# Performance work log

Hardware: AMD Instinct MI355X
Metric: run time of the kernel (lower is better)

The kernel has to match this reference:

```python
import jax, jax.numpy as jnp
import numpy as np

D_MODEL = 1024
N_HEADS = 16
D_K = D_MODEL // N_HEADS
D_FF = 4096
EPS = 1e-6


def _layernorm(x, g, b):
    mu = jnp.mean(x, axis=-1, keepdims=True)
    var = jnp.mean(jnp.square(x - mu), axis=-1, keepdims=True)
    return (x - mu) * jax.lax.rsqrt(var + EPS) * g + b


def setup_inputs() -> dict:
    key = jax.random.key(0)
    ks = jax.random.split(key, 12)
    B, S = 2, 2048
    sd_attn = (1.0 / np.sqrt(2.0)) * np.sqrt(2.0 / (D_MODEL + D_MODEL))  # xavier gain 1/sqrt(2) (std approx)
    sd_ff1 = np.sqrt(2.0 / (D_MODEL + D_FF))
    sd_ff2 = np.sqrt(2.0 / (D_FF + D_MODEL))
    return {
        "x": jax.random.normal(ks[0], (B, S, D_MODEL), jnp.float32),
        "mask": jnp.ones((B, S), jnp.int32),
        # weights stored (in, out) so forward is x @ W
        "wq": jax.random.normal(ks[1], (D_MODEL, D_MODEL), jnp.float32) * sd_attn,
        "wk": jax.random.normal(ks[2], (D_MODEL, D_MODEL), jnp.float32) * sd_attn,
        "wv": jax.random.normal(ks[3], (D_MODEL, D_MODEL), jnp.float32) * sd_attn,
        "wo": jax.random.normal(ks[4], (D_MODEL, D_MODEL), jnp.float32) * sd_attn,
        "wo_b": jnp.zeros((D_MODEL,), jnp.float32),
        "w1": jax.random.normal(ks[5], (D_MODEL, D_FF), jnp.float32) * sd_ff1,
        "b1": jnp.zeros((D_FF,), jnp.float32),
        "w2": jax.random.normal(ks[6], (D_FF, D_MODEL), jnp.float32) * sd_ff2,
        "b2": jnp.zeros((D_MODEL,), jnp.float32),
        "g1": jnp.ones((D_MODEL,), jnp.float32),
        "be1": jnp.zeros((D_MODEL,), jnp.float32),
        "g2": jnp.ones((D_MODEL,), jnp.float32),
        "be2": jnp.zeros((D_MODEL,), jnp.float32),
    }


def reference(x, mask, wq, wk, wv, wo, wo_b, w1, b1, w2, b2, g1, be1, g2, be2):
    B, S, _ = x.shape
    scale = 1.0 / np.sqrt(D_K)
    # project and split heads -> [B, H, S, Dk]
    q = (x @ wq).reshape(B, S, N_HEADS, D_K).transpose(0, 2, 1, 3)
    k = (x @ wk).reshape(B, S, N_HEADS, D_K).transpose(0, 2, 1, 3)
    v = (x @ wv).reshape(B, S, N_HEADS, D_K).transpose(0, 2, 1, 3)
    scores = jnp.einsum("bhqd,bhkd->bhqk", q, k) * scale  # [B,H,S,S]
    m = (mask[:, None, None, :] == 0)
    scores = jnp.where(m, -1e9, scores)
    attn = jax.nn.softmax(scores, axis=-1)
    ctx = jnp.einsum("bhqk,bhkd->bhqd", attn, v)
    ctx = ctx.transpose(0, 2, 1, 3).reshape(B, S, D_MODEL)
    attn_out = ctx @ wo + wo_b
    x = _layernorm(x + attn_out, g1, be1)
    ff = jax.nn.gelu(x @ w1 + b1, approximate=False) @ w2 + b2
    return _layernorm(x + ff, g2, be2)
```

## Files before the change

kernel.cpp:

```cpp
#include <hip/hip_runtime.h>
#include <cstdint>

#define DEVINL __device__ __forceinline__

typedef __attribute__((ext_vector_type(8))) short short8;
typedef __attribute__((ext_vector_type(4))) short short4v;
typedef __attribute__((ext_vector_type(4))) float floatx4;
typedef __attribute__((ext_vector_type(4))) unsigned short ushort4v;

DEVINL uint32_t pkbf(float a, float b) {
  uint32_t d;
  asm("v_cvt_pk_bf16_f32 %0, %1, %2" : "=v"(d) : "v"(a), "v"(b));
  return d;
}
DEVINL unsigned short f2bf(float f) {
  union { float f; uint32_t u; } v; v.f = f;
  return (unsigned short)((v.u + 0x7fffu + ((v.u >> 16) & 1u)) >> 16);
}
DEVINL float bf2f(unsigned short h) {
  union { uint32_t u; float f; } v; v.u = ((uint32_t)h) << 16;
  return v.f;
}

#if defined(__has_builtin) && __has_builtin(__builtin_amdgcn_exp2f)
#define EXP2(x) __builtin_amdgcn_exp2f(x)
#else
#define EXP2(x) exp2f(x)
#endif

DEVINL float fast_gelu(float v) {
  const float z = -2.30220795f * v * (1.0f + 0.044715f * v * v);
  return v * __builtin_amdgcn_rcpf(1.0f + EXP2(z));
}

typedef __attribute__((address_space(3))) unsigned char* lds_ptr_t;
typedef const __attribute__((address_space(1))) unsigned char* gbl_ptr_t;
DEVINL void load_lds_128(const void* g, void* l) {
  __builtin_amdgcn_global_load_lds((gbl_ptr_t)g, (lds_ptr_t)l, 16, 0, 0);
}

#define MFMA16(a, b, c) __builtin_amdgcn_mfma_f32_16x16x32_bf16((a), (b), (c), 0, 0, 0)

#define QSCALE2 0.18033688011112042f

__global__ __launch_bounds__(256) void prep_kernel(
    const float* __restrict__ x, unsigned short* __restrict__ XB,
    const float* __restrict__ wq, const float* __restrict__ wk,
    const float* __restrict__ wv, const float* __restrict__ wo,
    unsigned short* __restrict__ WQKV, unsigned short* __restrict__ WOT,
    const float* __restrict__ w1, unsigned short* __restrict__ W1T,
    const float* __restrict__ w2, unsigned short* __restrict__ W2T,
    const int* __restrict__ mask, unsigned short* __restrict__ MB) {
  const int bid = blockIdx.x;
  if (bid >= 16384) {
    const int i0 = threadIdx.x * 16;
#pragma unroll
    for (int j = 0; j < 16; ++j) MB[i0 + j] = mask[i0 + j] ? 0x3F80 : 0;
    return;
  }
  if (bid < 4096) {
    const int i = (bid * 256 + threadIdx.x) * 4;
    floatx4 v = *(const floatx4*)(x + i);
    union { uint32_t u[2]; ushort4v v4; } o;
    o.u[0] = pkbf(v[0], v[1]);
    o.u[1] = pkbf(v[2], v[3]);
    *(ushort4v*)(XB + i) = o.v4;
    return;
  }
  const float* in;
  unsigned short* out;
  int K, N, bx, by;
  if (bid < 8192) {
    const int b2 = bid - 4096, z = b2 >> 10;
    in = (z == 0) ? wq : (z == 1) ? wk : (z == 2) ? wv : wo;
    out = (z == 3) ? WOT : WQKV + (size_t)z * 1024 * 1024;
    K = 1024; N = 1024; bx = b2 & 31; by = (b2 >> 5) & 31;
  } else if (bid < 12288) {
    const int b3 = bid - 8192;
    in = w1; out = W1T; K = 1024; N = 4096; bx = b3 & 127; by = b3 >> 7;
  } else {
    const int b4 = bid - 12288;
    in = w2; out = W2T; K = 4096; N = 1024; bx = b4 & 31; by = b4 >> 5;
  }
  __shared__ float tile[32][33];
  const int n0 = bx * 32, k0 = by * 32;
  const int tx = threadIdx.x & 31, ty = threadIdx.x >> 5;
#pragma unroll
  for (int i = 0; i < 4; ++i)
    tile[ty + 8 * i][tx] = in[(size_t)(k0 + ty + 8 * i) * N + n0 + tx];
  __syncthreads();
#pragma unroll
  for (int i = 0; i < 4; ++i)
    out[(size_t)(n0 + ty + 8 * i) * K + k0 + tx] = f2bf(tile[tx][ty + 8 * i]);
}

template <int EPI, int SK>
__global__ __launch_bounds__(256) void gemm_bt_kernel(
    const unsigned short* __restrict__ A, const unsigned short* __restrict__ BT,
    const float* __restrict__ bias, void* __restrict__ C0, void* __restrict__ C1,
    void* __restrict__ C2, int M, int N, int K, const int* __restrict__ msk) {
  __shared__ __align__(16) unsigned short As[128 * 64];
  __shared__ __align__(16) unsigned short Bs[128 * 64];
  const int tid = threadIdx.x;
  const int w = tid >> 6, l = tid & 63;
  const int lq = l >> 4, lr = l & 15;
  const int m0 = blockIdx.y * 128, n0 = blockIdx.x * 128;
  const int wm = (w >> 1) * 64, wn = (w & 1) * 64;
  const int r_a = l >> 2;
  const int colb = (l & 3) * 8;
  const int kslice = K / SK;
  const int kbeg = kslice * blockIdx.z;
  const int region = (EPI == 5) ? (n0 >> 10) : 0;

  uint32_t mbits = 0xFFFFu;
  if (EPI == 5 && region == 2) {
    mbits = 0;
#pragma unroll
    for (int mt = 0; mt < 4; ++mt) {
      const int4 m4 = *(const int4*)(msk + m0 + wm + mt * 16 + lq * 4);
      mbits |= (m4.x ? 1u : 0u) << (mt * 4);
      mbits |= (m4.y ? 1u : 0u) << (mt * 4 + 1);
      mbits |= (m4.z ? 1u : 0u) << (mt * 4 + 2);
      mbits |= (m4.w ? 1u : 0u) << (mt * 4 + 3);
    }
  }

  floatx4 acc[4][4];
  const floatx4 fz = {0.f, 0.f, 0.f, 0.f};
#pragma unroll
  for (int mt = 0; mt < 4; ++mt)
#pragma unroll
    for (int nt = 0; nt < 4; ++nt) acc[mt][nt] = fz;

  for (int k0 = kbeg; k0 < kbeg + kslice; k0 += 64) {
    __syncthreads();
#pragma unroll
    for (int p = 0; p < 2; ++p) {
#pragma unroll
      for (int i = 0; i < 2; ++i) {
        const int c = w * 2 + i;
        load_lds_128(A + (size_t)(m0 + c * 16 + r_a) * K + k0 + p * 32 + colb,
                     (char*)As + p * 8192 + c * 1024);
        load_lds_128(BT + (size_t)(n0 + c * 16 + r_a) * K + k0 + p * 32 + colb,
                     (char*)Bs + p * 8192 + c * 1024);
      }
    }
    __syncthreads();
#pragma unroll
    for (int p = 0; p < 2; ++p) {
      short8 af[4], bf[4];
#pragma unroll
      for (int mt = 0; mt < 4; ++mt)
        af[mt] = *(const short8*)((const char*)As + p * 8192 + (wm + mt * 16 + lr) * 64 + lq * 16);
#pragma unroll
      for (int nt = 0; nt < 4; ++nt)
        bf[nt] = *(const short8*)((const char*)Bs + p * 8192 + (wn + nt * 16 + lr) * 64 + lq * 16);
#pragma unroll
      for (int mt = 0; mt < 4; ++mt)
#pragma unroll
        for (int nt = 0; nt < 4; ++nt)
          acc[mt][nt] = MFMA16(af[mt], bf[nt], acc[mt][nt]);
    }
  }

  void* Cp = (SK > 1 && blockIdx.z) ? C1 : C0;
#pragma unroll
  for (int mt = 0; mt < 4; ++mt) {
#pragma unroll
    for (int nt = 0; nt < 4; ++nt) {
      const int n = n0 + wn + nt * 16 + lr;
      float bval = 0.f;
      if (EPI == 2) bval = bias[n];
#pragma unroll
      for (int r = 0; r < 4; ++r) {
        const int m = m0 + wm + mt * 16 + lq * 4 + r;
        float v = acc[mt][nt][r];
        if (EPI == 4) {
          ((unsigned short*)Cp)[(size_t)m * N + n] = f2bf(v);
        } else if (EPI == 2) {
          ((unsigned short*)C0)[(size_t)m * N + n] = f2bf(fast_gelu(v + bval));
        } else {
          if (region == 0) {
            ((unsigned short*)C0)[(size_t)m * 1024 + n] = f2bf(v * QSCALE2);
          } else if (region == 1) {
            ((unsigned short*)C1)[(size_t)m * 1024 + (n - 1024)] = f2bf(v);
          } else {
            const int nn = n - 2048;
            const int bidx = m >> 11, s = m & 2047;
            const int u = s & 31;
            const int sp = (s & ~31) | (u & 3) | (((u >> 4) & 1) << 2) | (((u >> 2) & 3) << 3);
            const int hh = nn >> 6, d = nn & 63;
            const float vv = ((mbits >> (mt * 4 + r)) & 1u) ? v : 0.f;
            ((unsigned short*)C2)[((size_t)((bidx * 16 + hh) * 64 + d)) * 2048 + sp] = f2bf(vv);
          }
        }
      }
    }
  }
}

__global__ __launch_bounds__(256, 4) void flash_kernel(
    const unsigned short* __restrict__ Q, const unsigned short* __restrict__ Kg,
    const unsigned short* __restrict__ VT, const unsigned short* __restrict__ MB,
    unsigned short* __restrict__ ctx) {
  __shared__ __align__(16) unsigned short Ks[128 * 64];
  __shared__ __align__(16) unsigned short VTs[64 * 128];

  const int tid = threadIdx.x, w = tid >> 6, l = tid & 63;
  const int lq = l >> 4, lr = l & 15;
  const int bh = blockIdx.y, b = bh >> 4, h = bh & 15;
  const int q0 = blockIdx.x * 64;

  const unsigned short* Qp = Q + (size_t)(b * 2048 + q0) * 1024 + h * 64;
  const unsigned short* Kp = Kg + (size_t)(b * 2048) * 1024 + h * 64;
  const unsigned short* VTp = VT + (size_t)bh * 64 * 2048;
  const unsigned short* mbp = MB + b * 2048;

  {
    const int rq = l >> 3, cs = l & 7;
#pragma unroll
    for (int i = 0; i < 2; ++i) {
      const int c = w * 2 + i;
      load_lds_128(Qp + (size_t)(c * 8 + rq) * 1024 + cs * 8, (char*)Ks + c * 1024);
    }
  }
  __syncthreads();
  short8 qf[2];
  qf[0] = *(const short8*)((const char*)Ks + (w * 16 + lr) * 128 + lq * 16);
  qf[1] = *(const short8*)((const char*)Ks + (w * 16 + lr) * 128 + 64 + lq * 16);

  const floatx4 fz = {0.f, 0.f, 0.f, 0.f};
  floatx4 o[4] = {fz, fz, fz, fz};
  floatx4 l_acc = fz;

  const int krow = l >> 3, kslot = l & 7;
  const int vrow = l >> 4, vslot = l & 15;

  for (int kb = 0; kb < 2048; kb += 128) {
    __syncthreads();
#pragma unroll
    for (int i = 0; i < 4; ++i) {
      const int c4 = w * 4 + i;
      {
        const int row = c4 * 8 + krow;
        const int cc = kslot ^ (row & 7);
        load_lds_128(Kp + (size_t)(kb + row) * 1024 + cc * 8, (char*)Ks + c4 * 1024);
      }
      {
        const int row = c4 * 4 + vrow;
        const int cc = vslot ^ (row & 15);
        load_lds_128(VTp + (size_t)row * 2048 + kb + cc * 8, (char*)VTs + c4 * 1024);
      }
    }
    short8 mf[4];
#pragma unroll
    for (int t = 0; t < 4; ++t) {
      const short4v ma = *(const short4v*)(mbp + kb + t * 32 + lq * 4);
      const short4v mb2 = *(const short4v*)(mbp + kb + t * 32 + 16 + lq * 4);
      mf[t] = short8{ma[0], ma[1], ma[2], ma[3], mb2[0], mb2[1], mb2[2], mb2[3]};
    }
    __syncthreads();

#pragma unroll
    for (int h2 = 0; h2 < 2; ++h2) {
      floatx4 s[4];
#pragma unroll
      for (int gg = 0; gg < 4; ++gg) {
        const int g = h2 * 4 + gg;
        const char* rowp = (const char*)Ks + (g * 16 + lr) * 128;
        short8 k0 = *(const short8*)(rowp + ((lq) ^ (lr & 7)) * 16);
        short8 k1 = *(const short8*)(rowp + ((4 + lq) ^ (lr & 7)) * 16);
        floatx4 t = MFMA16(k0, qf[0], fz);
        s[gg] = MFMA16(k1, qf[1], t);
      }
      short8 pf[2];
#pragma unroll
      for (int tt = 0; tt < 2; ++tt) {
        const floatx4 sL = s[tt * 2], sH = s[tt * 2 + 1];
        union { uint32_t u[4]; short8 s8; } pk;
        pk.u[0] = pkbf(EXP2(sL[0]), EXP2(sL[1]));
        pk.u[1] = pkbf(EXP2(sL[2]), EXP2(sL[3]));
        pk.u[2] = pkbf(EXP2(sH[0]), EXP2(sH[1]));
        pk.u[3] = pkbf(EXP2(sH[2]), EXP2(sH[3]));
        pf[tt] = pk.s8;
      }
#pragma unroll
      for (int tt = 0; tt < 2; ++tt) {
        const int t = h2 * 2 + tt;
        l_acc = MFMA16(pf[tt], mf[t], l_acc);
#pragma unroll
        for (int nt = 0; nt < 4; ++nt) {
          const int d = nt * 16 + lr;
          short8 vf = *(const short8*)((const char*)VTs + d * 256 +
                                       (((t * 4 + lq) ^ (d & 15)) * 16));
          o[nt] = MFMA16(pf[tt], vf, o[nt]);
        }
      }
    }
  }

#pragma unroll
  for (int r = 0; r < 4; ++r) {
    const float inv = 1.0f / l_acc[r];
    const int q = q0 + w * 16 + lq * 4 + r;
#pragma unroll
    for (int nt = 0; nt < 4; ++nt)
      ctx[(size_t)(b * 2048 + q) * 1024 + h * 64 + nt * 16 + lr] = f2bf(o[nt][r] * inv);
  }
}

template <int RESBF, int OUTBF>
__global__ __launch_bounds__(256) void ln2_kernel(
    const void* __restrict__ res, const unsigned short* __restrict__ y0,
    const unsigned short* __restrict__ y1, const float* __restrict__ bias,
    const float* __restrict__ gamma, const float* __restrict__ beta,
    void* __restrict__ outp) {
  const int row = blockIdx.x, t = threadIdx.x;
  const size_t base = (size_t)row * 1024 + t * 4;
  float v[4];
  if (RESBF) {
    ushort4v r4 = *(const ushort4v*)((const unsigned short*)res + base);
#pragma unroll
    for (int j = 0; j < 4; ++j) v[j] = bf2f(r4[j]);
  } else {
    floatx4 r4 = *(const floatx4*)((const float*)res + base);
#pragma unroll
    for (int j = 0; j < 4; ++j) v[j] = r4[j];
  }
  const ushort4v a4 = *(const ushort4v*)(y0 + base);
  const ushort4v b4v = *(const ushort4v*)(y1 + base);
  const floatx4 bi4 = *(const floatx4*)(bias + t * 4);
  float s = 0.f, ss = 0.f;
#pragma unroll
  for (int j = 0; j < 4; ++j) {
    v[j] += bf2f(a4[j]) + bf2f(b4v[j]) + bi4[j];
    s += v[j];
    ss += v[j] * v[j];
  }
#pragma unroll
  for (int off = 1; off < 64; off <<= 1) {
    s += __shfl_xor(s, off);
    ss += __shfl_xor(ss, off);
  }
  __shared__ float red[8];
  const int w = t >> 6;
  if ((t & 63) == 0) { red[w] = s; red[4 + w] = ss; }
  __syncthreads();
  s = red[0] + red[1] + red[2] + red[3];
  ss = red[4] + red[5] + red[6] + red[7];
  const float mean = s * (1.0f / 1024.0f);
  const float var = ss * (1.0f / 1024.0f) - mean * mean;
  const float rstd = rsqrtf(var + 1e-6f);
  const floatx4 g4 = *(const floatx4*)(gamma + t * 4);
  const floatx4 be4 = *(const floatx4*)(beta + t * 4);
  if (OUTBF) {
    union { uint32_t u[2]; ushort4v v4; } o;
    o.u[0] = pkbf((v[0] - mean) * rstd * g4[0] + be4[0],
                  (v[1] - mean) * rstd * g4[1] + be4[1]);
    o.u[1] = pkbf((v[2] - mean) * rstd * g4[2] + be4[2],
                  (v[3] - mean) * rstd * g4[3] + be4[3]);
    *(ushort4v*)((unsigned short*)outp + base) = o.v4;
  } else {
    floatx4 o;
#pragma unroll
    for (int j = 0; j < 4; ++j) o[j] = (v[j] - mean) * rstd * g4[j] + be4[j];
    *(floatx4*)((float*)outp + base) = o;
  }
}

extern "C" void kernel_launch(void* const* d_in, const int* in_sizes, int n_in,
                              void* d_out, int out_size, void* d_ws, size_t ws_size,
                              hipStream_t stream) {
  (void)in_sizes; (void)n_in; (void)out_size; (void)ws_size;
  const float* x    = (const float*)d_in[0];
  const int*   mask = (const int*)d_in[1];
  const float* wq   = (const float*)d_in[2];
  const float* wk   = (const float*)d_in[3];
  const float* wv   = (const float*)d_in[4];
  const float* wo   = (const float*)d_in[5];
  const float* wo_b = (const float*)d_in[6];
  const float* w1   = (const float*)d_in[7];
  const float* b1   = (const float*)d_in[8];
  const float* w2   = (const float*)d_in[9];
  const float* b2   = (const float*)d_in[10];
  const float* g1   = (const float*)d_in[11];
  const float* be1  = (const float*)d_in[12];
  const float* g2   = (const float*)d_in[13];
  const float* be2  = (const float*)d_in[14];
  float* out = (float*)d_out;

  char* ws = (char*)d_ws;
  const size_t MBy = 1024ull * 1024ull;
  unsigned short* WQKV = (unsigned short*)(ws + 0 * MBy);
  unsigned short* WOT  = (unsigned short*)(ws + 6 * MBy);
  unsigned short* W1T  = (unsigned short*)(ws + 8 * MBy);
  unsigned short* W2T  = (unsigned short*)(ws + 16 * MBy);
  unsigned short* XB   = (unsigned short*)(ws + 24 * MBy);
  unsigned short* Qb   = (unsigned short*)(ws + 32 * MBy);
  unsigned short* Kb   = (unsigned short*)(ws + 40 * MBy);
  unsigned short* VTb  = (unsigned short*)(ws + 48 * MBy);
  unsigned short* CTX  = (unsigned short*)(ws + 56 * MBy);
  unsigned short* ATT0 = (unsigned short*)(ws + 32 * MBy);
  unsigned short* ATT1 = (unsigned short*)(ws + 40 * MBy);
  unsigned short* Hb   = (unsigned short*)(ws + 24 * MBy);
  unsigned short* G1   = (unsigned short*)(ws + 32 * MBy);
  unsigned short* FF20 = (unsigned short*)(ws + 64 * MBy);
  unsigned short* FF21 = (unsigned short*)(ws + 72 * MBy);
  unsigned short* MB   = (unsigned short*)(ws + 78 * MBy);

  prep_kernel<<<16385, 256, 0, stream>>>(x, XB, wq, wk, wv, wo, WQKV, WOT,
                                         w1, W1T, w2, W2T, mask, MB);
  gemm_bt_kernel<5, 1><<<dim3(24, 32), 256, 0, stream>>>(
      XB, WQKV, nullptr, Qb, Kb, VTb, 4096, 3072, 1024, mask);
  flash_kernel<<<dim3(32, 32), 256, 0, stream>>>(Qb, Kb, VTb, MB, CTX);
  gemm_bt_kernel<4, 2><<<dim3(8, 32, 2), 256, 0, stream>>>(
      CTX, WOT, nullptr, ATT0, ATT1, nullptr, 4096, 1024, 1024, nullptr);
  ln2_kernel<0, 1><<<4096, 256, 0, stream>>>(x, ATT0, ATT1, wo_b, g1, be1, Hb);
  gemm_bt_kernel<2, 1><<<dim3(32, 32), 256, 0, stream>>>(
      Hb, W1T, b1, G1, nullptr, nullptr, 4096, 4096, 1024, nullptr);
  gemm_bt_kernel<4, 2><<<dim3(8, 32, 2), 256, 0, stream>>>(
      G1, W2T, nullptr, FF20, FF21, nullptr, 4096, 1024, 4096, nullptr);
  ln2_kernel<1, 0><<<4096, 256, 0, stream>>>(Hb, FF20, FF21, b2, g2, be2, out);
}
```

Baseline: 358.7 us.

## Use 32x32 MFMA with XOR-swizzled LDS in GEMM; remap flash blocks per XCD

The GEMM kernel switches from 16x16x32 to 32x32x16 bf16 MFMA tiles (2x2 per wave instead of 4x4), and XOR-swizzles the LDS column layout to avoid bank conflicts on the fragment reads. The epilogue row mapping and the mask bit packing are rewritten to match the 32x32 accumulator layout. Separately, the flash attention grid becomes 1D with an index remap so that the blocks of one batch-head land on the same XCD, which should improve L2 reuse of K/V. The larger MFMA reduces LDS reads per FLOP, but the per-element epilogue stores become more scattered.

```diff
diff --git a/kernel.cpp b/kernel.cpp
--- a/kernel.cpp
+++ b/kernel.cpp
@@ -6,6 +6,7 @@
 typedef __attribute__((ext_vector_type(8))) short short8;
 typedef __attribute__((ext_vector_type(4))) short short4v;
 typedef __attribute__((ext_vector_type(4))) float floatx4;
+typedef __attribute__((ext_vector_type(16))) float floatx16;
 typedef __attribute__((ext_vector_type(4))) unsigned short ushort4v;
 
 DEVINL uint32_t pkbf(float a, float b) {
@@ -40,6 +41,7 @@
 }
 
 #define MFMA16(a, b, c) __builtin_amdgcn_mfma_f32_16x16x32_bf16((a), (b), (c), 0, 0, 0)
+#define MFMA32(a, b, c) __builtin_amdgcn_mfma_f32_32x32x16_bf16((a), (b), (c), 0, 0, 0)
 
 #define QSCALE2 0.18033688011112042f
 
@@ -103,34 +105,39 @@
   __shared__ __align__(16) unsigned short Bs[128 * 64];
   const int tid = threadIdx.x;
   const int w = tid >> 6, l = tid & 63;
-  const int lq = l >> 4, lr = l & 15;
   const int m0 = blockIdx.y * 128, n0 = blockIdx.x * 128;
   const int wm = (w >> 1) * 64, wn = (w & 1) * 64;
-  const int r_a = l >> 2;
-  const int colb = (l & 3) * 8;
+  const int ml = l & 31;
+  const int hb = l >> 5;
+  const int r_c = l >> 2;
+  const int csl = l & 3;
+  const int cgl = (csl ^ (r_c & 3)) * 8;
   const int kslice = K / SK;
   const int kbeg = kslice * blockIdx.z;
   const int region = (EPI == 5) ? (n0 >> 10) : 0;
 
-  uint32_t mbits = 0xFFFFu;
+  uint32_t mb32[2] = {0xFFFFu, 0xFFFFu};
   if (EPI == 5 && region == 2) {
-    mbits = 0;
-#pragma unroll
-    for (int mt = 0; mt < 4; ++mt) {
-      const int4 m4 = *(const int4*)(msk + m0 + wm + mt * 16 + lq * 4);
-      mbits |= (m4.x ? 1u : 0u) << (mt * 4);
-      mbits |= (m4.y ? 1u : 0u) << (mt * 4 + 1);
-      mbits |= (m4.z ? 1u : 0u) << (mt * 4 + 2);
-      mbits |= (m4.w ? 1u : 0u) << (mt * 4 + 3);
-    }
-  }
-
-  floatx4 acc[4][4];
-  const floatx4 fz = {0.f, 0.f, 0.f, 0.f};
-#pragma unroll
-  for (int mt = 0; mt < 4; ++mt)
-#pragma unroll
-    for (int nt = 0; nt < 4; ++nt) acc[mt][nt] = fz;
+    mb32[0] = mb32[1] = 0;
+#pragma unroll
+    for (int mt = 0; mt < 2; ++mt)
+#pragma unroll
+      for (int g = 0; g < 4; ++g) {
+        const int4 m4 = *(const int4*)(msk + m0 + wm + mt * 32 + 4 * hb + 8 * g);
+        mb32[mt] |= (m4.x ? 1u : 0u) << (g * 4);
+        mb32[mt] |= (m4.y ? 1u : 0u) << (g * 4 + 1);
+        mb32[mt] |= (m4.z ? 1u : 0u) << (g * 4 + 2);
+        mb32[mt] |= (m4.w ? 1u : 0u) << (g * 4 + 3);
+      }
+  }
+
+  floatx16 acc[2][2];
+#pragma unroll
+  for (int mt = 0; mt < 2; ++mt)
+#pragma unroll
+    for (int nt = 0; nt < 2; ++nt)
+#pragma unroll
+      for (int r = 0; r < 16; ++r) acc[mt][nt][r] = 0.f;
 
   for (int k0 = kbeg; k0 < kbeg + kslice; k0 += 64) {
     __syncthreads();
@@ -139,42 +146,52 @@
 #pragma unroll
       for (int i = 0; i < 2; ++i) {
         const int c = w * 2 + i;
-        load_lds_128(A + (size_t)(m0 + c * 16 + r_a) * K + k0 + p * 32 + colb,
+        load_lds_128(A + (size_t)(m0 + c * 16 + r_c) * K + k0 + p * 32 + cgl,
                      (char*)As + p * 8192 + c * 1024);
-        load_lds_128(BT + (size_t)(n0 + c * 16 + r_a) * K + k0 + p * 32 + colb,
+        load_lds_128(BT + (size_t)(n0 + c * 16 + r_c) * K + k0 + p * 32 + cgl,
                      (char*)Bs + p * 8192 + c * 1024);
       }
     }
     __syncthreads();
 #pragma unroll
     for (int p = 0; p < 2; ++p) {
-      short8 af[4], bf[4];
-#pragma unroll
-      for (int mt = 0; mt < 4; ++mt)
-        af[mt] = *(const short8*)((const char*)As + p * 8192 + (wm + mt * 16 + lr) * 64 + lq * 16);
-#pragma unroll
-      for (int nt = 0; nt < 4; ++nt)
-        bf[nt] = *(const short8*)((const char*)Bs + p * 8192 + (wn + nt * 16 + lr) * 64 + lq * 16);
-#pragma unroll
-      for (int mt = 0; mt < 4; ++mt)
-#pragma unroll
-        for (int nt = 0; nt < 4; ++nt)
-          acc[mt][nt] = MFMA16(af[mt], bf[nt], acc[mt][nt]);
+#pragma unroll
+      for (int ks = 0; ks < 2; ++ks) {
+        short8 af[2], bf[2];
+        const int lc = ks * 2 + hb;
+#pragma unroll
+        for (int mt = 0; mt < 2; ++mt) {
+          const int row = wm + mt * 32 + ml;
+          af[mt] = *(const short8*)((const char*)As + p * 8192 + row * 64 +
+                                    ((lc ^ (row & 3)) * 16));
+        }
+#pragma unroll
+        for (int nt = 0; nt < 2; ++nt) {
+          const int row = wn + nt * 32 + ml;
+          bf[nt] = *(const short8*)((const char*)Bs + p * 8192 + row * 64 +
+                                    ((lc ^ (row & 3)) * 16));
+        }
+#pragma unroll
+        for (int mt = 0; mt < 2; ++mt)
+#pragma unroll
+          for (int nt = 0; nt < 2; ++nt)
+            acc[mt][nt] = MFMA32(af[mt], bf[nt], acc[mt][nt]);
+      }
     }
   }
 
   void* Cp = (SK > 1 && blockIdx.z) ? C1 : C0;
 #pragma unroll
-  for (int mt = 0; mt < 4; ++mt) {
-#pragma unroll
-    for (int nt = 0; nt < 4; ++nt) {
-      const int n = n0 + wn + nt * 16 + lr;
+  for (int mt = 0; mt < 2; ++mt) {
+#pragma unroll
+    for (int nt = 0; nt < 2; ++nt) {
+      const int n = n0 + wn + nt * 32 + ml;
       float bval = 0.f;
       if (EPI == 2) bval = bias[n];
 #pragma unroll
-      for (int r = 0; r < 4; ++r) {
-        const int m = m0 + wm + mt * 16 + lq * 4 + r;
-        float v = acc[mt][nt][r];
+      for (int reg = 0; reg < 16; ++reg) {
+        const int m = m0 + wm + mt * 32 + 4 * hb + (reg & 3) + 8 * (reg >> 2);
+        float v = acc[mt][nt][reg];
         if (EPI == 4) {
           ((unsigned short*)Cp)[(size_t)m * N + n] = f2bf(v);
         } else if (EPI == 2) {
@@ -190,7 +207,7 @@
             const int u = s & 31;
             const int sp = (s & ~31) | (u & 3) | (((u >> 4) & 1) << 2) | (((u >> 2) & 3) << 3);
             const int hh = nn >> 6, d = nn & 63;
-            const float vv = ((mbits >> (mt * 4 + r)) & 1u) ? v : 0.f;
+            const float vv = ((mb32[mt] >> reg) & 1u) ? v : 0.f;
             ((unsigned short*)C2)[((size_t)((bidx * 16 + hh) * 64 + d)) * 2048 + sp] = f2bf(vv);
           }
         }
@@ -208,8 +225,11 @@
 
   const int tid = threadIdx.x, w = tid >> 6, l = tid & 63;
   const int lq = l >> 4, lr = l & 15;
-  const int bh = blockIdx.y, b = bh >> 4, h = bh & 15;
-  const int q0 = blockIdx.x * 64;
+  const int lin = blockIdx.x;
+  const int xcd = lin & 7, slot = lin >> 3;
+  const int bh = xcd * 4 + (slot >> 5);
+  const int b = bh >> 4, h = bh & 15;
+  const int q0 = (slot & 31) * 64;
 
   const unsigned short* Qp = Q + (size_t)(b * 2048 + q0) * 1024 + h * 64;
   const unsigned short* Kp = Kg + (size_t)(b * 2048) * 1024 + h * 64;
@@ -412,7 +432,7 @@
                                          w1, W1T, w2, W2T, mask, MB);
   gemm_bt_kernel<5, 1><<<dim3(24, 32), 256, 0, stream>>>(
       XB, WQKV, nullptr, Qb, Kb, VTb, 4096, 3072, 1024, mask);
-  flash_kernel<<<dim3(32, 32), 256, 0, stream>>>(Qb, Kb, VTb, MB, CTX);
+  flash_kernel<<<1024, 256, 0, stream>>>(Qb, Kb, VTb, MB, CTX);
   gemm_bt_kernel<4, 2><<<dim3(8, 32, 2), 256, 0, stream>>>(
       CTX, WOT, nullptr, ATT0, ATT1, nullptr, 4096, 1024, 1024, nullptr);
   ln2_kernel<0, 1><<<4096, 256, 0, stream>>>(x, ATT0, ATT1, wo_b, g1, be1, Hb);
```

Measured after the change: 356.8 us. Within noise of the previous version (-0.5%).
